# Kernel tuning notes

Measured on AMD Instinct MI355X. Metric: run time of the kernel, lower is better.

The kernel has to match this reference:

```python
import jax, jax.numpy as jnp
import numpy as np

LUT_DIM = 33  # standard 33^3 color LUT


def setup_inputs() -> dict:
    key = jax.random.key(0)
    k1, k2 = jax.random.split(key)
    # learned 3D LUT: [out_channels=3, D_b, D_g, D_r]
    lut = jax.random.normal(k1, (3, LUT_DIM, LUT_DIM, LUT_DIM), dtype=jnp.float32) * 0.1
    # input image batch in [0, 1): [B, 3, H, W]
    x = jax.random.uniform(k2, (4, 3, 1024, 1024), dtype=jnp.float32)
    return {"lut": lut, "x": x}


def reference(lut, x):
    """Trilinear interpolation of a 3D color LUT (image-adaptive-3DLUT forward).

    lut: [3, D, D, D] laid out as lut[c, ib, ig, ir] (flat index ir + ig*D + ib*D*D)
    x:   [B, 3, H, W] with channels (r, g, b) in [0, 1]
    returns: [B, 3, H, W]
    """
    dim = lut.shape[-1]
    scale = dim - 1  # 1 / binsize

    r, g, b = x[:, 0], x[:, 1], x[:, 2]  # each [B, H, W]

    def cell(c):
        s = c * scale
        idx = jnp.clip(jnp.floor(s), 0, scale - 1).astype(jnp.int32)
        return idx, s - idx.astype(s.dtype)  # integer cell, fractional offset

    ir, dr = cell(r)
    ig, dg = cell(g)
    ib, db = cell(b)

    lut_flat = lut.reshape(3, -1)  # [3, D^3], tiny and cache-resident

    out = jnp.zeros((3,) + r.shape, dtype=x.dtype)  # [3, B, H, W]
    # 8 corners of the enclosing LUT cell, trilinear weights
    for or_ in (0, 1):
        wr = dr if or_ else (1.0 - dr)
        for og in (0, 1):
            wg = dg if og else (1.0 - dg)
            for ob in (0, 1):
                wb = db if ob else (1.0 - db)
                flat = ((ib + ob) * dim + (ig + og)) * dim + (ir + or_)  # [B, H, W]
                corner = lut_flat[:, flat]  # gather -> [3, B, H, W]
                out = out + (wr * wg * wb)[None] * corner

    return jnp.transpose(out, (1, 0, 2, 3))  # [B, 3, H, W]
```

## Files before the change

kernel.cpp:

```cpp
#include <hip/hip_runtime.h>


#define LUT_D   33
#define LUT_N   (LUT_D * LUT_D * LUT_D)
#define HW      (1024 * 1024)
#define HW4     (HW / 4)
#define NGROUPS (4 * HW4)
#define NCHUNKS 256
#define GROUPS_PER_BLOCK (NGROUPS / NCHUNKS)
#define THREADS 1024
#define ITERS   (GROUPS_PER_BLOCK / THREADS)

__global__ __launch_bounds__(THREADS)
void lut3d_trilerp_kernel(const float* __restrict__ lut,
                          const float* __restrict__ x,
                          float* __restrict__ out) {
    extern __shared__ float slut[];

    const int bx    = blockIdx.x;
    const int c     = bx % 3;
    const int chunk = bx / 3;

    const float* lc = lut + c * LUT_N;
    for (int i = threadIdx.x; i < LUT_N; i += THREADS) {
        slut[i] = lc[i];
    }
    __syncthreads();

    const float4* x4 = (const float4*)x;
    float4*       o4 = (float4*)out;

    const int g0 = chunk * GROUPS_PER_BLOCK + (int)threadIdx.x;

#pragma unroll
    for (int it = 0; it < ITERS; ++it) {
        const int g     = g0 + it * THREADS;
        const int b_img = g >> 18;
        const int hw4   = g & (HW4 - 1);
        const int ibase = b_img * 3 * HW4 + hw4;

        const float4 r4 = x4[ibase];
        const float4 g4 = x4[ibase + HW4];
        const float4 b4 = x4[ibase + 2 * HW4];

        const float rr[4] = {r4.x, r4.y, r4.z, r4.w};
        const float gg[4] = {g4.x, g4.y, g4.z, g4.w};
        const float bb[4] = {b4.x, b4.y, b4.z, b4.w};
        float oo[4];

#pragma unroll
        for (int k = 0; k < 4; ++k) {
            const float sr = rr[k] * 32.0f;
            const float sg = gg[k] * 32.0f;
            const float sb = bb[k] * 32.0f;
            float fr = fminf(fmaxf(floorf(sr), 0.0f), 31.0f);
            float fg = fminf(fmaxf(floorf(sg), 0.0f), 31.0f);
            float fb = fminf(fmaxf(floorf(sb), 0.0f), 31.0f);
            const float dr = sr - fr;
            const float dg = sg - fg;
            const float db = sb - fb;
            const int ir = (int)fr, ig = (int)fg, ib = (int)fb;
            const int idx = (ib * LUT_D + ig) * LUT_D + ir;

            const float v000 = slut[idx];
            const float v001 = slut[idx + 1];
            const float v010 = slut[idx + LUT_D];
            const float v011 = slut[idx + LUT_D + 1];
            const float v100 = slut[idx + LUT_D * LUT_D];
            const float v101 = slut[idx + LUT_D * LUT_D + 1];
            const float v110 = slut[idx + LUT_D * LUT_D + LUT_D];
            const float v111 = slut[idx + LUT_D * LUT_D + LUT_D + 1];

            const float l00 = v000 + dr * (v001 - v000);
            const float l01 = v010 + dr * (v011 - v010);
            const float l10 = v100 + dr * (v101 - v100);
            const float l11 = v110 + dr * (v111 - v110);
            const float l0  = l00 + dg * (l01 - l00);
            const float l1  = l10 + dg * (l11 - l10);
            oo[k] = l0 + db * (l1 - l0);
        }

        o4[(b_img * 3 + c) * HW4 + hw4] = make_float4(oo[0], oo[1], oo[2], oo[3]);
    }
}

extern "C" void kernel_launch(void* const* d_in, const int* in_sizes, int n_in,
                              void* d_out, int out_size, void* d_ws, size_t ws_size,
                              hipStream_t stream) {
    const float* lut = (const float*)d_in[0];
    const float* x   = (const float*)d_in[1];
    float*       out = (float*)d_out;

    const int grid = 3 * NCHUNKS;
    const size_t lds_bytes = LUT_N * sizeof(float);

    lut3d_trilerp_kernel<<<grid, THREADS, lds_bytes, stream>>>(lut, x, out);
}
```

Measured before the change: 120.8 us.

## Repack LUT into per-cell fp16 corner blocks and interpolate with packed dot products

A pre-pass kernel repacks the LUT into a global table with one 48-byte record per cell, holding the 8 corners of all 3 channels as fp16 pairs. The main kernel then fetches a cell with three 16-byte loads and computes each output channel with four fdot2 instructions. The old per-channel blocks that staged the LUT in LDS and read the input three times are replaced by one pass that emits all three channels, using nontemporal stores. This removes the threefold input re-read and the LDS staging, but depends on the L2 for the 1.5 MB cell table. It also lowers the LUT values and trilinear weights to fp16, which costs accuracy.

```diff
diff --git a/kernel.cpp b/kernel.cpp
--- a/kernel.cpp
+++ b/kernel.cpp
@@ -1,87 +1,132 @@
 #include <hip/hip_runtime.h>
+#include <hip/hip_fp16.h>
 
 
-#define LUT_D   33
-#define LUT_N   (LUT_D * LUT_D * LUT_D)
-#define HW      (1024 * 1024)
-#define HW4     (HW / 4)
-#define NGROUPS (4 * HW4)
-#define NCHUNKS 256
-#define GROUPS_PER_BLOCK (NGROUPS / NCHUNKS)
-#define THREADS 1024
-#define ITERS   (GROUPS_PER_BLOCK / THREADS)
+#define LUT_D  33
+#define LUT_DD (LUT_D * LUT_D)
+#define LUT_N  (LUT_D * LUT_D * LUT_D)
+#define HW4    (1024 * 1024 / 4)
+#define NG     (4 * HW4)
+#define CELLS  (32 * 32 * 32)
 
-__global__ __launch_bounds__(THREADS)
-void lut3d_trilerp_kernel(const float* __restrict__ lut,
-                          const float* __restrict__ x,
-                          float* __restrict__ out) {
-    extern __shared__ float slut[];
+typedef _Float16 half2v  __attribute__((ext_vector_type(2)));
+typedef __fp16   fp16x2  __attribute__((ext_vector_type(2)));
+typedef float    vfloat4 __attribute__((ext_vector_type(4)));
 
-    const int bx    = blockIdx.x;
-    const int c     = bx % 3;
-    const int chunk = bx / 3;
+__device__ __align__(64) unsigned int g_cells[CELLS * 16];
 
-    const float* lc = lut + c * LUT_N;
-    for (int i = threadIdx.x; i < LUT_N; i += THREADS) {
-        slut[i] = lc[i];
+union U32H2 { unsigned int u; half2v h; fp16x2 f; __half2 hh; };
+
+__device__ __forceinline__ half2v as_h2(unsigned int u) {
+    U32H2 cv; cv.u = u; return cv.h;
+}
+
+__device__ __forceinline__ half2v pk_h2(float a, float b) {
+    U32H2 cv; cv.f = __builtin_amdgcn_cvt_pkrtz(a, b);
+    return cv.h;
+}
+
+__device__ __forceinline__ float dot_h2(half2v a, half2v b, float acc) {
+    return __builtin_amdgcn_fdot2(a, b, acc, false);
+}
+
+__global__ __launch_bounds__(256)
+void cell_pack_kernel(const float* __restrict__ lut) {
+    const int id = blockIdx.x * 256 + (int)threadIdx.x;
+    const int ir = id & 31;
+    const int ig = (id >> 5) & 31;
+    const int ib = id >> 10;
+    const int base = (ib * LUT_D + ig) * LUT_D + ir;
+
+    unsigned int w[12];
+#pragma unroll
+    for (int c = 0; c < 3; ++c) {
+        const float* L = lut + c * LUT_N + base;
+#pragma unroll
+        for (int ob = 0; ob < 2; ++ob) {
+#pragma unroll
+            for (int og = 0; og < 2; ++og) {
+                const float* p = L + ob * LUT_DD + og * LUT_D;
+                U32H2 cv; cv.hh = __floats2half2_rn(p[0], p[1]);
+                w[c * 4 + ob * 2 + og] = cv.u;
+            }
+        }
     }
-    __syncthreads();
+    uint4* dst = (uint4*)(g_cells + (id << 4));
+    dst[0] = make_uint4(w[0], w[1], w[2],  w[3]);
+    dst[1] = make_uint4(w[4], w[5], w[6],  w[7]);
+    dst[2] = make_uint4(w[8], w[9], w[10], w[11]);
+}
+
+__global__ __launch_bounds__(256)
+void lut3d_cell_kernel(const float* __restrict__ x, float* __restrict__ out) {
+    const int g     = blockIdx.x * 256 + (int)threadIdx.x;
+    const int b_img = g >> 18;
+    const int hw4   = g & (HW4 - 1);
+    const int ibase = b_img * 3 * HW4 + hw4;
 
     const float4* x4 = (const float4*)x;
     float4*       o4 = (float4*)out;
 
-    const int g0 = chunk * GROUPS_PER_BLOCK + (int)threadIdx.x;
+    const float4 r4 = x4[ibase];
+    const float4 g4 = x4[ibase + HW4];
+    const float4 b4 = x4[ibase + 2 * HW4];
+
+    const float RR[4] = {r4.x, r4.y, r4.z, r4.w};
+    const float GG[4] = {g4.x, g4.y, g4.z, g4.w};
+    const float BB[4] = {b4.x, b4.y, b4.z, b4.w};
+    float o0[4], o1[4], o2[4];
 
 #pragma unroll
-    for (int it = 0; it < ITERS; ++it) {
-        const int g     = g0 + it * THREADS;
-        const int b_img = g >> 18;
-        const int hw4   = g & (HW4 - 1);
-        const int ibase = b_img * 3 * HW4 + hw4;
+    for (int k = 0; k < 4; ++k) {
+        const float sr = RR[k] * 32.0f;
+        const float sg = GG[k] * 32.0f;
+        const float sb = BB[k] * 32.0f;
+        const float fr = fminf(fmaxf(floorf(sr), 0.0f), 31.0f);
+        const float fg = fminf(fmaxf(floorf(sg), 0.0f), 31.0f);
+        const float fb = fminf(fmaxf(floorf(sb), 0.0f), 31.0f);
+        const float dr = sr - fr;
+        const float dg = sg - fg;
+        const float db = sb - fb;
 
-        const float4 r4 = x4[ibase];
-        const float4 g4 = x4[ibase + HW4];
-        const float4 b4 = x4[ibase + 2 * HW4];
+        const int cell = ((int)fb << 10) | ((int)fg << 5) | (int)fr;
+        const uint4* cp = (const uint4*)(g_cells + (cell << 4));
+        const uint4 q0 = cp[0];
+        const uint4 q1 = cp[1];
+        const uint4 q2 = cp[2];
 
-        const float rr[4] = {r4.x, r4.y, r4.z, r4.w};
-        const float gg[4] = {g4.x, g4.y, g4.z, g4.w};
-        const float bb[4] = {b4.x, b4.y, b4.z, b4.w};
-        float oo[4];
+        const float wr0 = 1.0f - dr;
+        const float wg0 = 1.0f - dg;
+        const float wb0 = 1.0f - db;
+        const float p00 = wb0 * wg0;
+        const float p01 = wb0 * dg;
+        const float p10 = db  * wg0;
+        const float p11 = db  * dg;
+        const half2v w0 = pk_h2(p00 * wr0, p00 * dr);
+        const half2v w1 = pk_h2(p01 * wr0, p01 * dr);
+        const half2v w2 = pk_h2(p10 * wr0, p10 * dr);
+        const half2v w3 = pk_h2(p11 * wr0, p11 * dr);
 
-#pragma unroll
-        for (int k = 0; k < 4; ++k) {
-            const float sr = rr[k] * 32.0f;
-            const float sg = gg[k] * 32.0f;
-            const float sb = bb[k] * 32.0f;
-            float fr = fminf(fmaxf(floorf(sr), 0.0f), 31.0f);
-            float fg = fminf(fmaxf(floorf(sg), 0.0f), 31.0f);
-            float fb = fminf(fmaxf(floorf(sb), 0.0f), 31.0f);
-            const float dr = sr - fr;
-            const float dg = sg - fg;
-            const float db = sb - fb;
-            const int ir = (int)fr, ig = (int)fg, ib = (int)fb;
-            const int idx = (ib * LUT_D + ig) * LUT_D + ir;
+        o0[k] = dot_h2(as_h2(q0.x), w0,
+                dot_h2(as_h2(q0.y), w1,
+                dot_h2(as_h2(q0.z), w2,
+                dot_h2(as_h2(q0.w), w3, 0.0f))));
+        o1[k] = dot_h2(as_h2(q1.x), w0,
+                dot_h2(as_h2(q1.y), w1,
+                dot_h2(as_h2(q1.z), w2,
+                dot_h2(as_h2(q1.w), w3, 0.0f))));
+        o2[k] = dot_h2(as_h2(q2.x), w0,
+                dot_h2(as_h2(q2.y), w1,
+                dot_h2(as_h2(q2.z), w2,
+                dot_h2(as_h2(q2.w), w3, 0.0f))));
+    }
 
-            const float v000 = slut[idx];
-            const float v001 = slut[idx + 1];
-            const float v010 = slut[idx + LUT_D];
-            const float v011 = slut[idx + LUT_D + 1];
-            const float v100 = slut[idx + LUT_D * LUT_D];
-            const float v101 = slut[idx + LUT_D * LUT_D + 1];
-            const float v110 = slut[idx + LUT_D * LUT_D + LUT_D];
-            const float v111 = slut[idx + LUT_D * LUT_D + LUT_D + 1];
-
-            const float l00 = v000 + dr * (v001 - v000);
-            const float l01 = v010 + dr * (v011 - v010);
-            const float l10 = v100 + dr * (v101 - v100);
-            const float l11 = v110 + dr * (v111 - v110);
-            const float l0  = l00 + dg * (l01 - l00);
-            const float l1  = l10 + dg * (l11 - l10);
-            oo[k] = l0 + db * (l1 - l0);
-        }
-
-        o4[(b_img * 3 + c) * HW4 + hw4] = make_float4(oo[0], oo[1], oo[2], oo[3]);
-    }
+    vfloat4 v0 = {o0[0], o0[1], o0[2], o0[3]};
+    vfloat4 v1 = {o1[0], o1[1], o1[2], o1[3]};
+    vfloat4 v2 = {o2[0], o2[1], o2[2], o2[3]};
+    __builtin_nontemporal_store(v0, (vfloat4*)&o4[ibase]);
+    __builtin_nontemporal_store(v1, (vfloat4*)&o4[ibase + HW4]);
+    __builtin_nontemporal_store(v2, (vfloat4*)&o4[ibase + 2 * HW4]);
 }
 
 extern "C" void kernel_launch(void* const* d_in, const int* in_sizes, int n_in,
@@ -91,8 +136,6 @@
     const float* x   = (const float*)d_in[1];
     float*       out = (float*)d_out;
 
-    const int grid = 3 * NCHUNKS;
-    const size_t lds_bytes = LUT_N * sizeof(float);
-
-    lut3d_trilerp_kernel<<<grid, THREADS, lds_bytes, stream>>>(lut, x, out);
+    cell_pack_kernel<<<CELLS / 256, 256, 0, stream>>>(lut);
+    lut3d_cell_kernel<<<NG / 256, 256, 0, stream>>>(x, out);
 }
```

Measured after the change: 139.2 us. +15.2%, slower.
